# Performance work log

Hardware: AMD Instinct MI355X
Metric: run time of the kernel (lower is better)

## Reference

```python
import jax, jax.numpy as jnp
import numpy as np

B, A, UNITS, HID, T = 16, 256, 64, 64, 3


def setup_inputs() -> dict:
    key = jax.random.key(0)
    ks = jax.random.split(key, 16)
    x = jax.random.normal(ks[0], (B, A + 2, A), dtype=jnp.float32)
    # GNN message-passing weights (torch.randn in original)
    W0 = jax.random.normal(ks[1], (1, UNITS), dtype=jnp.float32)
    W1 = jax.random.normal(ks[2], (UNITS, UNITS), dtype=jnp.float32)
    W2 = jax.random.normal(ks[3], (UNITS, UNITS), dtype=jnp.float32)
    W3 = jax.random.normal(ks[4], (1, UNITS), dtype=jnp.float32)
    # fc_a: Linear(64,64)->ReLU->Linear(64,32)->ReLU->Linear(32,1); stored (in,out)
    s = lambda k, i, o: jax.random.uniform(k, (i, o), jnp.float32, -1, 1) / np.sqrt(i)
    sb = lambda k, i, o: jax.random.uniform(k, (o,), jnp.float32, -1, 1) / np.sqrt(i)
    a_w1, a_b1 = s(ks[5], UNITS, HID), sb(ks[6], UNITS, HID)
    a_w2, a_b2 = s(ks[7], HID, HID // 2), sb(ks[8], HID, HID // 2)
    a_w3, a_b3 = s(ks[9], HID // 2, 1), sb(ks[10], HID // 2, 1)
    # fc_v: Linear(64,64)->ReLU->Linear(64,1)
    v_w1, v_b1 = s(ks[11], UNITS, HID), sb(ks[12], UNITS, HID)
    v_w2, v_b2 = s(ks[13], HID, 1), sb(ks[14], HID, 1)
    return dict(x=x, W0=W0, W1=W1, W2=W2, W3=W3,
                a_w1=a_w1, a_b1=a_b1, a_w2=a_w2, a_b2=a_b2, a_w3=a_w3, a_b3=a_b3,
                v_w1=v_w1, v_b1=v_b1, v_w2=v_w2, v_b2=v_b2)


def reference(x, W0, W1, W2, W3,
              a_w1, a_b1, a_w2, a_b2, a_w3, a_b3,
              v_w1, v_b1, v_w2, v_b2):
    n_actions = x.shape[2]                       # A
    cur_sol = x[:, 0, :][..., None]              # [B, A, 1]
    mask = x[:, 1, :]                            # [B, A]
    weights = x[:, 2:n_actions + 2, :]           # [B, A, A]
    adjacent = (weights != 0).astype(jnp.float32)
    embedding = jnp.zeros((x.shape[0], n_actions, UNITS), dtype=jnp.float32)

    # e3 is loop-invariant in math, but original recomputes each step; keep T small python loop (faithful, T=3 static)
    for _ in range(T):
        e1 = cur_sol @ W0                                        # [B,A,1]@[1,U] -> [B,A,U]
        e2 = (adjacent @ embedding / n_actions) @ W1             # [B,A,U]
        # weights.reshape(B,A,A,1) @ W3(1,U) == outer-product broadcast
        e3_ = jnp.sum(jax.nn.relu(weights[..., None] * W3[0]), axis=2) / n_actions  # [B,A,U]
        e3 = e3_ @ W2
        embedding = jax.nn.relu(e1 + e2 + e3)

    # dueling heads
    h = jax.nn.relu(embedding @ a_w1 + a_b1)
    h = jax.nn.relu(h @ a_w2 + a_b2)
    out_a = (h @ a_w3 + a_b3)[..., 0]                            # [B, A]
    hv = jax.nn.relu(embedding @ v_w1 + v_b1)
    out_v = (hv @ v_w2 + v_b2)[..., 0]                           # [B, A]
    out_v = jnp.sum(out_v, axis=1, keepdims=True)                # [B, 1]
    output = out_v + (out_a - jnp.sum(out_a, axis=1, keepdims=True))
    output = output + mask * 10.0                                # hard_mask=False
    return output
```

## Files before the change

### kernel.cpp

```cpp
#include <hip/hip_runtime.h>


#define NB 16
#define NA 256
#define NU 64

__device__ __forceinline__ float reluf(float v) { return fmaxf(v, 0.f); }

__global__ __launch_bounds__(256) void k_fused(
    const float* __restrict__ x,
    const float* __restrict__ W0, const float* __restrict__ W1,
    const float* __restrict__ W2, const float* __restrict__ W3,
    const float* __restrict__ aw1, const float* __restrict__ ab1,
    const float* __restrict__ aw2, const float* __restrict__ ab2,
    const float* __restrict__ aw3, const float* __restrict__ ab3,
    const float* __restrict__ vw1, const float* __restrict__ vb1,
    const float* __restrict__ vw2, const float* __restrict__ vb2,
    float* __restrict__ oaw, float* __restrict__ partA, float* __restrict__ partV,
    unsigned int* __restrict__ cnt, float* __restrict__ embg,
    float* __restrict__ out)
{
    __shared__ float bufA[12384];
    __shared__ float W1s[4096];
    __shared__ unsigned long long zmsL[1024];
    __shared__ float poss[256], negs[256], css[256];
    __shared__ float W0s[64], P2s[64], N2s[64], Ssh[64], e2c[64];
    __shared__ float wpart[256], npart[256];
    __shared__ int   zrow[256];
    __shared__ int   zw[4];
    __shared__ float ab1s[64], vb1s[64], vw2s[64], ab2s[32], aw3s[32];
    __shared__ float ab3s[1], vb2s[1];
    __shared__ float soa[32], sov[32];
    __shared__ int   slast;

    const float invA = 1.0f / 256.0f;
    const int t = threadIdx.x;
    const int batch = blockIdx.x & 15;
    const int sub   = blockIdx.x >> 4;
    const int obase = sub * 32;
    float* aw1s = bufA;
    float* vw1s = bufA + 4096;
    float* aw2s = bufA + 8192;
    float* embs = bufA + 10304;

    #pragma unroll
    for (int k = 0; k < 4; ++k) {
        int idx = k * 1024 + t * 4;
        *(float4*)&aw1s[idx] = *(const float4*)&aw1[idx];
        *(float4*)&vw1s[idx] = *(const float4*)&vw1[idx];
        *(float4*)&W1s[idx]  = *(const float4*)&W1[idx];
    }
    #pragma unroll
    for (int k = 0; k < 8; ++k) {
        int idx = k * 256 + t;
        aw2s[(idx >> 5) * 33 + (idx & 31)] = aw2[idx];
    }
    if (t < 64) { W0s[t] = W0[t]; ab1s[t] = ab1[t]; vb1s[t] = vb1[t]; vw2s[t] = vw2[t]; }
    if (t >= 64 && t < 96) { ab2s[t - 64] = ab2[t - 64]; aw3s[t - 64] = aw3[t - 64]; }
    if (t == 96) { ab3s[0] = ab3[0]; vb2s[0] = vb2[0]; }

    {
        const int r4 = t >> 2, sub4 = t & 3;
        #pragma unroll
        for (int p = 0; p < 4; ++p) {
            int row = p * 64 + r4;
            const float* rowp = x + ((size_t)batch * 258 + 2 + row) * 256 + sub4 * 64;
            float pp = 0.f, nn = 0.f;
            int zf = 0;
            #pragma unroll
            for (int c = 0; c < 64; c += 4) {
                float4 v = *(const float4*)(rowp + c);
                pp += fmaxf(v.x, 0.f) + fmaxf(v.y, 0.f) + fmaxf(v.z, 0.f) + fmaxf(v.w, 0.f);
                nn += fminf(v.x, 0.f) + fminf(v.y, 0.f) + fminf(v.z, 0.f) + fminf(v.w, 0.f);
                zf |= (v.x == 0.f) | (v.y == 0.f) | (v.z == 0.f) | (v.w == 0.f);
            }
            pp += __shfl_xor(pp, 1); pp += __shfl_xor(pp, 2);
            nn += __shfl_xor(nn, 1); nn += __shfl_xor(nn, 2);
            zf |= __shfl_xor(zf, 1); zf |= __shfl_xor(zf, 2);
            if (sub4 == 0) { poss[row] = pp; negs[row] = nn; zrow[row] = zf; }
        }
        css[t] = x[(size_t)batch * 66048 + t];
    }

    {
        int j = t & 63, mg = t >> 6;
        float pa = 0.f, na = 0.f;
        #pragma unroll
        for (int k = 0; k < 16; ++k) {
            int m = mg * 16 + k;
            float w3 = W3[m];
            float w2 = W2[m * 64 + j];
            pa = fmaf(fmaxf(w3, 0.f), w2, pa);
            na = fmaf(fminf(w3, 0.f), w2, na);
        }
        wpart[mg * 64 + j] = pa;
        npart[mg * 64 + j] = na;
    }
    __syncthreads();
    {
        if (t < 64) {
            P2s[t] = wpart[t] + wpart[64 + t] + wpart[128 + t] + wpart[192 + t];
            N2s[t] = npart[t] + npart[64 + t] + npart[128 + t] + npart[192 + t];
        }
        int zf = zrow[t];
        unsigned long long ball = __ballot(zf != 0);
        if ((t & 63) == 0) zw[t >> 6] = (ball != 0ull) ? 1 : 0;
    }
    __syncthreads();
    const int dirty = zw[0] | zw[1] | zw[2] | zw[3];

    if (!dirty) {
        const int j = t & 63, rg = t >> 6;
        const float w0j = W0s[j], p2j = P2s[j], n2j = N2s[j];
        float c_j = 0.f;
        #pragma unroll
        for (int iter = 0; iter < 2; ++iter) {
            float s = 0.f;
            #pragma unroll 8
            for (int k = 0; k < 64; ++k) {
                int i = rg * 64 + k;
                s += reluf(fmaf(css[i], w0j, (poss[i] * p2j + negs[i] * n2j) * invA) + c_j);
            }
            wpart[rg * 64 + j] = s;
            __syncthreads();
            if (t < 64) {
                float S = wpart[t] + wpart[64 + t] + wpart[128 + t] + wpart[192 + t];
                Ssh[t] = S;
                float c = 0.f;
                #pragma unroll 8
                for (int m = 0; m < 64; ++m) c = fmaf(Ssh[m], W1s[m * 64 + t], c);
                e2c[t] = c * invA;
            }
            __syncthreads();
            c_j = e2c[j];
        }
        #pragma unroll
        for (int k = 0; k < 8; ++k) {
            int idx = k * 256 + t;
            int il = idx >> 6, j2 = idx & 63;
            int row = obase + il;
            embs[il * 65 + j2] = reluf(fmaf(css[row], W0s[j2],
                                 (poss[row] * P2s[j2] + negs[row] * N2s[j2]) * invA)
                                 + e2c[j2]);
        }
    } else {
        {
            const int r4 = t >> 2, sub4 = t & 3;
            #pragma unroll
            for (int p = 0; p < 4; ++p) {
                int row = p * 64 + r4;
                unsigned long long zm = 0ull;
                if (zrow[row]) {
                    const float* rowp = x + ((size_t)batch * 258 + 2 + row) * 256 + sub4 * 64;
                    for (int c = 0; c < 64; ++c)
                        if (rowp[c] == 0.f) zm |= 1ull << c;
                }
                zmsL[row * 4 + sub4] = zm;
            }
        }
        __syncthreads();
        float* eb0 = embg + (size_t)blockIdx.x * 32768;
        float* eb1 = eb0 + 16384;
        const int r4 = t >> 2, sub4 = t & 3, jb = sub4 * 16;
        #pragma unroll
        for (int p = 0; p < 4; ++p) {
            int row = p * 64 + r4;
            float cs = css[row], pi = poss[row], ni = negs[row];
            #pragma unroll
            for (int q = 0; q < 16; ++q) {
                int jj = jb + q;
                eb0[row * 64 + jj] = reluf(fmaf(cs, W0s[jj],
                                      (pi * P2s[jj] + ni * N2s[jj]) * invA));
            }
        }
        __syncthreads();
        float* cur = eb0; float* nxt = eb1;
        for (int it = 1; it <= 2; ++it) {
            {
                int j = t & 63, rg = t >> 6;
                float s = 0.f;
                for (int k = 0; k < 64; ++k) s += cur[(rg * 64 + k) * 64 + j];
                wpart[rg * 64 + j] = s;
            }
            __syncthreads();
            if (t < 64) {
                float S = wpart[t] + wpart[64 + t] + wpart[128 + t] + wpart[192 + t];
                Ssh[t] = S;
                float c = 0.f;
                for (int m = 0; m < 64; ++m) c = fmaf(Ssh[m], W1s[m * 64 + t], c);
                e2c[t] = c * invA;
            }
            __syncthreads();
            #pragma unroll
            for (int p = 0; p < 4; ++p) {
                int row = p * 64 + r4;
                float cs = css[row], pi = poss[row], ni = negs[row];
                float acc[16];
                #pragma unroll
                for (int q = 0; q < 16; ++q) {
                    int jj = jb + q;
                    acc[q] = fmaf(cs, W0s[jj], (pi * P2s[jj] + ni * N2s[jj]) * invA)
                             + e2c[jj];
                }
                if (zrow[row]) {
                    for (int wd = 0; wd < 4; ++wd) {
                        unsigned long long zm = zmsL[row * 4 + wd];
                        while (zm) {
                            int k = wd * 64 + __builtin_ctzll(zm);
                            zm &= zm - 1;
                            float corr[16];
                            #pragma unroll
                            for (int q = 0; q < 16; ++q) corr[q] = 0.f;
                            for (int m = 0; m < 64; ++m) {
                                float ebm = cur[k * 64 + m];
                                #pragma unroll
                                for (int q = 0; q < 16; ++q)
                                    corr[q] = fmaf(ebm, W1s[m * 64 + jb + q], corr[q]);
                            }
                            #pragma unroll
                            for (int q = 0; q < 16; ++q) acc[q] -= corr[q] * invA;
                        }
                    }
                }
                #pragma unroll
                for (int q = 0; q < 16; ++q)
                    nxt[row * 64 + jb + q] = reluf(acc[q]);
            }
            __syncthreads();
            float* tmp = cur; cur = nxt; nxt = tmp;
        }
        #pragma unroll
        for (int k = 0; k < 8; ++k) {
            int idx = k * 256 + t;
            int il = idx >> 6, j2 = idx & 63;
            embs[il * 65 + j2] = cur[(obase + il) * 64 + j2];
        }
    }
    __syncthreads();

    const int lr = t >> 3;
    const int jb = (t & 7) * 8;

    float h1[8], hv[8];
    #pragma unroll
    for (int q = 0; q < 8; ++q) { h1[q] = ab1s[jb + q]; hv[q] = vb1s[jb + q]; }

    for (int m = 0; m < 64; ++m) {
        float em = embs[lr * 65 + m];
        const float4 a0 = *(const float4*)&aw1s[m * 64 + jb];
        const float4 a1 = *(const float4*)&aw1s[m * 64 + jb + 4];
        const float4 b0 = *(const float4*)&vw1s[m * 64 + jb];
        const float4 b1 = *(const float4*)&vw1s[m * 64 + jb + 4];
        h1[0] = fmaf(em, a0.x, h1[0]); h1[1] = fmaf(em, a0.y, h1[1]);
        h1[2] = fmaf(em, a0.z, h1[2]); h1[3] = fmaf(em, a0.w, h1[3]);
        h1[4] = fmaf(em, a1.x, h1[4]); h1[5] = fmaf(em, a1.y, h1[5]);
        h1[6] = fmaf(em, a1.z, h1[6]); h1[7] = fmaf(em, a1.w, h1[7]);
        hv[0] = fmaf(em, b0.x, hv[0]); hv[1] = fmaf(em, b0.y, hv[1]);
        hv[2] = fmaf(em, b0.z, hv[2]); hv[3] = fmaf(em, b0.w, hv[3]);
        hv[4] = fmaf(em, b1.x, hv[4]); hv[5] = fmaf(em, b1.y, hv[5]);
        hv[6] = fmaf(em, b1.z, hv[6]); hv[7] = fmaf(em, b1.w, hv[7]);
    }

    float ovp = 0.f;
    #pragma unroll
    for (int q = 0; q < 8; ++q) {
        h1[q] = reluf(h1[q]);
        hv[q] = reluf(hv[q]);
        ovp = fmaf(hv[q], vw2s[jb + q], ovp);
    }
    ovp += __shfl_xor(ovp, 1); ovp += __shfl_xor(ovp, 2); ovp += __shfl_xor(ovp, 4);

    float h2p[32];
    #pragma unroll
    for (int j2 = 0; j2 < 32; ++j2) h2p[j2] = 0.f;
    #pragma unroll
    for (int q = 0; q < 8; ++q) {
        float h = h1[q];
        int rr = jb + q;
        #pragma unroll
        for (int j2 = 0; j2 < 32; ++j2) h2p[j2] = fmaf(h, aw2s[rr * 33 + j2], h2p[j2]);
    }
    #pragma unroll
    for (int j2 = 0; j2 < 32; ++j2) {
        float s = h2p[j2];
        s += __shfl_xor(s, 1); s += __shfl_xor(s, 2); s += __shfl_xor(s, 4);
        h2p[j2] = s;
    }

    if ((t & 7) == 0) {
        float oa = ab3s[0];
        #pragma unroll
        for (int j2 = 0; j2 < 32; ++j2)
            oa = fmaf(reluf(h2p[j2] + ab2s[j2]), aw3s[j2], oa);
        __hip_atomic_store(&oaw[batch * 256 + obase + lr], oa,
                           __ATOMIC_RELAXED, __HIP_MEMORY_SCOPE_AGENT);
        soa[lr] = oa;
        sov[lr] = ovp + vb2s[0];
    }
    __syncthreads();
    if (t < 32) {
        float a = soa[t], v = sov[t];
        a += __shfl_xor(a, 1); a += __shfl_xor(a, 2); a += __shfl_xor(a, 4);
        a += __shfl_xor(a, 8); a += __shfl_xor(a, 16);
        v += __shfl_xor(v, 1); v += __shfl_xor(v, 2); v += __shfl_xor(v, 4);
        v += __shfl_xor(v, 8); v += __shfl_xor(v, 16);
        if (t == 0) {
            __hip_atomic_store(&partA[blockIdx.x], a,
                               __ATOMIC_RELAXED, __HIP_MEMORY_SCOPE_AGENT);
            __hip_atomic_store(&partV[blockIdx.x], v,
                               __ATOMIC_RELAXED, __HIP_MEMORY_SCOPE_AGENT);
        }
    }

    __syncthreads();
    if (t == 0) {
        unsigned int old = __hip_atomic_fetch_add(&cnt[batch], 1u,
                               __ATOMIC_ACQ_REL, __HIP_MEMORY_SCOPE_AGENT);
        slast = (((old + 1u) & 7u) == 0u);
    }
    __syncthreads();
    if (slast) {
        float oa = __hip_atomic_load(&oaw[batch * 256 + t],
                                     __ATOMIC_RELAXED, __HIP_MEMORY_SCOPE_AGENT);
        float sA = 0.f, sV = 0.f;
        #pragma unroll
        for (int k = 0; k < 8; ++k) {
            sA += __hip_atomic_load(&partA[k * 16 + batch],
                                    __ATOMIC_RELAXED, __HIP_MEMORY_SCOPE_AGENT);
            sV += __hip_atomic_load(&partV[k * 16 + batch],
                                    __ATOMIC_RELAXED, __HIP_MEMORY_SCOPE_AGENT);
        }
        float mask = x[((size_t)batch * 258 + 1) * 256 + t];
        out[batch * 256 + t] = sV + oa - sA + mask * 10.0f;
    }
}

extern "C" void kernel_launch(void* const* d_in, const int* in_sizes, int n_in,
                              void* d_out, int out_size, void* d_ws, size_t ws_size,
                              hipStream_t stream)
{
    (void)in_sizes; (void)n_in; (void)out_size; (void)ws_size;
    const float* x   = (const float*)d_in[0];
    const float* W0  = (const float*)d_in[1];
    const float* W1  = (const float*)d_in[2];
    const float* W2  = (const float*)d_in[3];
    const float* W3  = (const float*)d_in[4];
    const float* aw1 = (const float*)d_in[5];
    const float* ab1 = (const float*)d_in[6];
    const float* aw2 = (const float*)d_in[7];
    const float* ab2 = (const float*)d_in[8];
    const float* aw3 = (const float*)d_in[9];
    const float* ab3 = (const float*)d_in[10];
    const float* vw1 = (const float*)d_in[11];
    const float* vb1 = (const float*)d_in[12];
    const float* vw2 = (const float*)d_in[13];
    const float* vb2 = (const float*)d_in[14];

    float* ws    = (float*)d_ws;
    float* oaw   = ws;
    float* partA = ws + 4096;
    float* partV = ws + 4224;
    unsigned int* cnt = (unsigned int*)(ws + 4352);
    float* embg  = ws + 8192;

    k_fused<<<128, 256, 0, stream>>>(x, W0, W1, W2, W3,
                                     aw1, ab1, aw2, ab2, aw3, ab3,
                                     vw1, vb1, vw2, vb2,
                                     oaw, partA, partV, cnt, embg, (float*)d_out);
}
```

Measured before the change: 28.86 us.

## Split row-statistics scan across blocks and exchange via global flags

```diff
diff --git a/kernel.cpp b/kernel.cpp
--- a/kernel.cpp
+++ b/kernel.cpp
@@ -1,9 +1,9 @@
 #include <hip/hip_runtime.h>
 
 
-#define NB 16
-#define NA 256
-#define NU 64
+#define MC  0x5F3A9C71u
+#define MD  0x5F3A9C72u
+#define MDN 0x5F3A9C73u
 
 __device__ __forceinline__ float reluf(float v) { return fmaxf(v, 0.f); }
 
@@ -16,71 +16,59 @@
     const float* __restrict__ aw3, const float* __restrict__ ab3,
     const float* __restrict__ vw1, const float* __restrict__ vb1,
     const float* __restrict__ vw2, const float* __restrict__ vb2,
-    float* __restrict__ oaw, float* __restrict__ partA, float* __restrict__ partV,
-    unsigned int* __restrict__ cnt, float* __restrict__ embg,
-    float* __restrict__ out)
+    float* __restrict__ oaw, float* __restrict__ ovv,
+    float* __restrict__ possg, float* __restrict__ negsg,
+    unsigned int* __restrict__ flagg, unsigned int* __restrict__ flag2,
+    float* __restrict__ embg, float* __restrict__ out)
 {
-    __shared__ float bufA[12384];
-    __shared__ float W1s[4096];
-    __shared__ unsigned long long zmsL[1024];
+    __shared__ float aw1s[4096], vw1s[4096], W1s[4096];
+    __shared__ float aw2s[64 * 36];
+    __shared__ float embsT[64 * 36];
     __shared__ float poss[256], negs[256], css[256];
     __shared__ float W0s[64], P2s[64], N2s[64], Ssh[64], e2c[64];
     __shared__ float wpart[256], npart[256];
-    __shared__ int   zrow[256];
-    __shared__ int   zw[4];
     __shared__ float ab1s[64], vb1s[64], vw2s[64], ab2s[32], aw3s[32];
-    __shared__ float ab3s[1], vb2s[1];
-    __shared__ float soa[32], sov[32];
-    __shared__ int   slast;
+    __shared__ float ab3s[1], vb2s[1], sov[32];
+    __shared__ int zw[4];
+    __shared__ unsigned int sflags[8];
+    __shared__ int zrow[256];
+    __shared__ unsigned long long zmsL[1024];
 
     const float invA = 1.0f / 256.0f;
     const int t = threadIdx.x;
     const int batch = blockIdx.x & 15;
     const int sub   = blockIdx.x >> 4;
     const int obase = sub * 32;
-    float* aw1s = bufA;
-    float* vw1s = bufA + 4096;
-    float* aw2s = bufA + 8192;
-    float* embs = bufA + 10304;
-
-    #pragma unroll
-    for (int k = 0; k < 4; ++k) {
-        int idx = k * 1024 + t * 4;
-        *(float4*)&aw1s[idx] = *(const float4*)&aw1[idx];
-        *(float4*)&vw1s[idx] = *(const float4*)&vw1[idx];
-        *(float4*)&W1s[idx]  = *(const float4*)&W1[idx];
-    }
-    #pragma unroll
-    for (int k = 0; k < 8; ++k) {
-        int idx = k * 256 + t;
-        aw2s[(idx >> 5) * 33 + (idx & 31)] = aw2[idx];
-    }
-    if (t < 64) { W0s[t] = W0[t]; ab1s[t] = ab1[t]; vb1s[t] = vb1[t]; vw2s[t] = vw2[t]; }
-    if (t >= 64 && t < 96) { ab2s[t - 64] = ab2[t - 64]; aw3s[t - 64] = aw3[t - 64]; }
-    if (t == 96) { ab3s[0] = ab3[0]; vb2s[0] = vb2[0]; }
 
     {
-        const int r4 = t >> 2, sub4 = t & 3;
+        int r8 = t >> 3, s8 = t & 7;
+        int grow = obase + r8;
+        const float* rowp = x + ((size_t)batch * 258 + 2 + grow) * 256 + s8 * 32;
+        float pp = 0.f, nn = 0.f, mn = 1e30f;
         #pragma unroll
-        for (int p = 0; p < 4; ++p) {
-            int row = p * 64 + r4;
-            const float* rowp = x + ((size_t)batch * 258 + 2 + row) * 256 + sub4 * 64;
-            float pp = 0.f, nn = 0.f;
-            int zf = 0;
-            #pragma unroll
-            for (int c = 0; c < 64; c += 4) {
-                float4 v = *(const float4*)(rowp + c);
-                pp += fmaxf(v.x, 0.f) + fmaxf(v.y, 0.f) + fmaxf(v.z, 0.f) + fmaxf(v.w, 0.f);
-                nn += fminf(v.x, 0.f) + fminf(v.y, 0.f) + fminf(v.z, 0.f) + fminf(v.w, 0.f);
-                zf |= (v.x == 0.f) | (v.y == 0.f) | (v.z == 0.f) | (v.w == 0.f);
-            }
-            pp += __shfl_xor(pp, 1); pp += __shfl_xor(pp, 2);
-            nn += __shfl_xor(nn, 1); nn += __shfl_xor(nn, 2);
-            zf |= __shfl_xor(zf, 1); zf |= __shfl_xor(zf, 2);
-            if (sub4 == 0) { poss[row] = pp; negs[row] = nn; zrow[row] = zf; }
-        }
-        css[t] = x[(size_t)batch * 66048 + t];
-    }
+        for (int c = 0; c < 32; c += 4) {
+            float4 v = *(const float4*)(rowp + c);
+            pp += fmaxf(v.x, 0.f) + fmaxf(v.y, 0.f) + fmaxf(v.z, 0.f) + fmaxf(v.w, 0.f);
+            nn += fminf(v.x, 0.f) + fminf(v.y, 0.f) + fminf(v.z, 0.f) + fminf(v.w, 0.f);
+            mn = fminf(mn, fminf(fminf(fabsf(v.x), fabsf(v.y)),
+                                 fminf(fabsf(v.z), fabsf(v.w))));
+        }
+        pp += __shfl_xor(pp, 1); pp += __shfl_xor(pp, 2); pp += __shfl_xor(pp, 4);
+        nn += __shfl_xor(nn, 1); nn += __shfl_xor(nn, 2); nn += __shfl_xor(nn, 4);
+        mn = fminf(mn, __shfl_xor(mn, 1));
+        mn = fminf(mn, __shfl_xor(mn, 2));
+        mn = fminf(mn, __shfl_xor(mn, 4));
+        if (s8 == 0) {
+            __hip_atomic_store(&possg[batch * 256 + grow], pp,
+                               __ATOMIC_RELAXED, __HIP_MEMORY_SCOPE_AGENT);
+            __hip_atomic_store(&negsg[batch * 256 + grow], nn,
+                               __ATOMIC_RELAXED, __HIP_MEMORY_SCOPE_AGENT);
+        }
+        int z = (s8 == 0 && mn == 0.f) ? 1 : 0;
+        unsigned long long b = __ballot(z);
+        if ((t & 63) == 0) zw[t >> 6] = (b != 0ull);
+    }
+    css[t] = x[(size_t)batch * 66048 + t];
 
     {
         int j = t & 63, mg = t >> 6;
@@ -97,17 +85,51 @@
         npart[mg * 64 + j] = na;
     }
     __syncthreads();
-    {
-        if (t < 64) {
-            P2s[t] = wpart[t] + wpart[64 + t] + wpart[128 + t] + wpart[192 + t];
-            N2s[t] = npart[t] + npart[64 + t] + npart[128 + t] + npart[192 + t];
-        }
-        int zf = zrow[t];
-        unsigned long long ball = __ballot(zf != 0);
-        if ((t & 63) == 0) zw[t >> 6] = (ball != 0ull) ? 1 : 0;
-    }
-    __syncthreads();
-    const int dirty = zw[0] | zw[1] | zw[2] | zw[3];
+    if (t == 0) {
+        unsigned int fv = (zw[0] | zw[1] | zw[2] | zw[3]) ? MD : MC;
+        __hip_atomic_store(&flagg[blockIdx.x], fv,
+                           __ATOMIC_RELEASE, __HIP_MEMORY_SCOPE_AGENT);
+    }
+    if (t < 64) {
+        P2s[t] = wpart[t] + wpart[64 + t] + wpart[128 + t] + wpart[192 + t];
+        N2s[t] = npart[t] + npart[64 + t] + npart[128 + t] + npart[192 + t];
+    }
+
+    #pragma unroll
+    for (int k = 0; k < 4; ++k) {
+        int idx = k * 1024 + t * 4;
+        *(float4*)&aw1s[idx] = *(const float4*)&aw1[idx];
+        *(float4*)&vw1s[idx] = *(const float4*)&vw1[idx];
+        *(float4*)&W1s[idx]  = *(const float4*)&W1[idx];
+    }
+    #pragma unroll
+    for (int k = 0; k < 8; ++k) {
+        int idx = k * 256 + t;
+        aw2s[(idx >> 5) * 36 + (idx & 31)] = aw2[idx];
+    }
+    if (t < 64) { W0s[t] = W0[t]; ab1s[t] = ab1[t]; vb1s[t] = vb1[t]; vw2s[t] = vw2[t]; }
+    if (t >= 64 && t < 96) { ab2s[t - 64] = ab2[t - 64]; aw3s[t - 64] = aw3[t - 64]; }
+    if (t == 96) { ab3s[0] = ab3[0]; vb2s[0] = vb2[0]; }
+
+    if (t < 8) {
+        const unsigned int* f = &flagg[t * 16 + batch];
+        unsigned int v = __hip_atomic_load(f, __ATOMIC_ACQUIRE, __HIP_MEMORY_SCOPE_AGENT);
+        while (v != MC && v != MD) {
+            __builtin_amdgcn_s_sleep(1);
+            v = __hip_atomic_load(f, __ATOMIC_ACQUIRE, __HIP_MEMORY_SCOPE_AGENT);
+        }
+        sflags[t] = v;
+    }
+    __syncthreads();
+    const int dirty = (sflags[0] == MD) | (sflags[1] == MD) | (sflags[2] == MD) |
+                      (sflags[3] == MD) | (sflags[4] == MD) | (sflags[5] == MD) |
+                      (sflags[6] == MD) | (sflags[7] == MD);
+
+    poss[t] = __hip_atomic_load(&possg[batch * 256 + t],
+                                __ATOMIC_RELAXED, __HIP_MEMORY_SCOPE_AGENT);
+    negs[t] = __hip_atomic_load(&negsg[batch * 256 + t],
+                                __ATOMIC_RELAXED, __HIP_MEMORY_SCOPE_AGENT);
+    __syncthreads();
 
     if (!dirty) {
         const int j = t & 63, rg = t >> 6;
@@ -134,14 +156,16 @@
             __syncthreads();
             c_j = e2c[j];
         }
-        #pragma unroll
-        for (int k = 0; k < 8; ++k) {
-            int idx = k * 256 + t;
-            int il = idx >> 6, j2 = idx & 63;
-            int row = obase + il;
-            embs[il * 65 + j2] = reluf(fmaf(css[row], W0s[j2],
-                                 (poss[row] * P2s[j2] + negs[row] * N2s[j2]) * invA)
-                                 + e2c[j2]);
+        {
+            int r = t & 31, mg = t >> 5;
+            int grow = obase + r;
+            float cs = css[grow], pi = poss[grow], ni = negs[grow];
+            #pragma unroll
+            for (int jj = 0; jj < 8; ++jj) {
+                int m = mg * 8 + jj;
+                embsT[m * 36 + r] = reluf(fmaf(cs, W0s[m],
+                                    (pi * P2s[m] + ni * N2s[m]) * invA) + e2c[m]);
+            }
         }
     } else {
         {
@@ -149,13 +173,14 @@
             #pragma unroll
             for (int p = 0; p < 4; ++p) {
                 int row = p * 64 + r4;
+                const float* rowp = x + ((size_t)batch * 258 + 2 + row) * 256 + sub4 * 64;
                 unsigned long long zm = 0ull;
-                if (zrow[row]) {
-                    const float* rowp = x + ((size_t)batch * 258 + 2 + row) * 256 + sub4 * 64;
-                    for (int c = 0; c < 64; ++c)
-                        if (rowp[c] == 0.f) zm |= 1ull << c;
-                }
+                for (int c = 0; c < 64; ++c)
+                    if (rowp[c] == 0.f) zm |= 1ull << c;
                 zmsL[row * 4 + sub4] = zm;
+                int zf = (zm != 0ull);
+                zf |= __shfl_xor(zf, 1); zf |= __shfl_xor(zf, 2);
+                if (sub4 == 0) zrow[row] = zf;
             }
         }
         __syncthreads();
@@ -229,107 +254,114 @@
             __syncthreads();
             float* tmp = cur; cur = nxt; nxt = tmp;
         }
-        #pragma unroll
-        for (int k = 0; k < 8; ++k) {
-            int idx = k * 256 + t;
-            int il = idx >> 6, j2 = idx & 63;
-            embs[il * 65 + j2] = cur[(obase + il) * 64 + j2];
-        }
-    }
-    __syncthreads();
-
-    const int lr = t >> 3;
-    const int jb = (t & 7) * 8;
-
-    float h1[8], hv[8];
+        for (int idx = t; idx < 2048; idx += 256) {
+            int r = idx & 31, m = idx >> 5;
+            embsT[m * 36 + r] = cur[(obase + r) * 64 + m];
+        }
+    }
+    __syncthreads();
+
+    const int cg  = t & 31;
+    const int rg4 = t >> 5;
+    float aA0x = 0.f, aA0y = 0.f, aA1x = 0.f, aA1y = 0.f;
+    float aA2x = 0.f, aA2y = 0.f, aA3x = 0.f, aA3y = 0.f;
+    float aV0x = 0.f, aV0y = 0.f, aV1x = 0.f, aV1y = 0.f;
+    float aV2x = 0.f, aV2y = 0.f, aV3x = 0.f, aV3y = 0.f;
+    for (int m = 0; m < 64; ++m) {
+        float4 em = *(const float4*)&embsT[m * 36 + rg4 * 4];
+        float2 a2 = *(const float2*)&aw1s[m * 64 + 2 * cg];
+        float2 v2 = *(const float2*)&vw1s[m * 64 + 2 * cg];
+        aA0x = fmaf(em.x, a2.x, aA0x); aA0y = fmaf(em.x, a2.y, aA0y);
+        aA1x = fmaf(em.y, a2.x, aA1x); aA1y = fmaf(em.y, a2.y, aA1y);
+        aA2x = fmaf(em.z, a2.x, aA2x); aA2y = fmaf(em.z, a2.y, aA2y);
+        aA3x = fmaf(em.w, a2.x, aA3x); aA3y = fmaf(em.w, a2.y, aA3y);
+        aV0x = fmaf(em.x, v2.x, aV0x); aV0y = fmaf(em.x, v2.y, aV0y);
+        aV1x = fmaf(em.y, v2.x, aV1x); aV1y = fmaf(em.y, v2.y, aV1y);
+        aV2x = fmaf(em.z, v2.x, aV2x); aV2y = fmaf(em.z, v2.y, aV2y);
+        aV3x = fmaf(em.w, v2.x, aV3x); aV3y = fmaf(em.w, v2.y, aV3y);
+    }
+    float wvx = vw2s[2 * cg], wvy = vw2s[2 * cg + 1];
+    float pv0 = fmaf(reluf(aV0x + vb1s[2 * cg]), wvx, reluf(aV0y + vb1s[2 * cg + 1]) * wvy);
+    float pv1 = fmaf(reluf(aV1x + vb1s[2 * cg]), wvx, reluf(aV1y + vb1s[2 * cg + 1]) * wvy);
+    float pv2 = fmaf(reluf(aV2x + vb1s[2 * cg]), wvx, reluf(aV2y + vb1s[2 * cg + 1]) * wvy);
+    float pv3 = fmaf(reluf(aV3x + vb1s[2 * cg]), wvx, reluf(aV3y + vb1s[2 * cg + 1]) * wvy);
     #pragma unroll
-    for (int q = 0; q < 8; ++q) { h1[q] = ab1s[jb + q]; hv[q] = vb1s[jb + q]; }
-
-    for (int m = 0; m < 64; ++m) {
-        float em = embs[lr * 65 + m];
-        const float4 a0 = *(const float4*)&aw1s[m * 64 + jb];
-        const float4 a1 = *(const float4*)&aw1s[m * 64 + jb + 4];
-        const float4 b0 = *(const float4*)&vw1s[m * 64 + jb];
-        const float4 b1 = *(const float4*)&vw1s[m * 64 + jb + 4];
-        h1[0] = fmaf(em, a0.x, h1[0]); h1[1] = fmaf(em, a0.y, h1[1]);
-        h1[2] = fmaf(em, a0.z, h1[2]); h1[3] = fmaf(em, a0.w, h1[3]);
-        h1[4] = fmaf(em, a1.x, h1[4]); h1[5] = fmaf(em, a1.y, h1[5]);
-        h1[6] = fmaf(em, a1.z, h1[6]); h1[7] = fmaf(em, a1.w, h1[7]);
-        hv[0] = fmaf(em, b0.x, hv[0]); hv[1] = fmaf(em, b0.y, hv[1]);
-        hv[2] = fmaf(em, b0.z, hv[2]); hv[3] = fmaf(em, b0.w, hv[3]);
-        hv[4] = fmaf(em, b1.x, hv[4]); hv[5] = fmaf(em, b1.y, hv[5]);
-        hv[6] = fmaf(em, b1.z, hv[6]); hv[7] = fmaf(em, b1.w, hv[7]);
-    }
-
-    float ovp = 0.f;
-    #pragma unroll
-    for (int q = 0; q < 8; ++q) {
-        h1[q] = reluf(h1[q]);
-        hv[q] = reluf(hv[q]);
-        ovp = fmaf(hv[q], vw2s[jb + q], ovp);
-    }
-    ovp += __shfl_xor(ovp, 1); ovp += __shfl_xor(ovp, 2); ovp += __shfl_xor(ovp, 4);
-
-    float h2p[32];
-    #pragma unroll
-    for (int j2 = 0; j2 < 32; ++j2) h2p[j2] = 0.f;
-    #pragma unroll
-    for (int q = 0; q < 8; ++q) {
-        float h = h1[q];
-        int rr = jb + q;
-        #pragma unroll
-        for (int j2 = 0; j2 < 32; ++j2) h2p[j2] = fmaf(h, aw2s[rr * 33 + j2], h2p[j2]);
-    }
-    #pragma unroll
-    for (int j2 = 0; j2 < 32; ++j2) {
-        float s = h2p[j2];
-        s += __shfl_xor(s, 1); s += __shfl_xor(s, 2); s += __shfl_xor(s, 4);
-        h2p[j2] = s;
-    }
-
-    if ((t & 7) == 0) {
-        float oa = ab3s[0];
-        #pragma unroll
-        for (int j2 = 0; j2 < 32; ++j2)
-            oa = fmaf(reluf(h2p[j2] + ab2s[j2]), aw3s[j2], oa);
-        __hip_atomic_store(&oaw[batch * 256 + obase + lr], oa,
+    for (int mk = 1; mk <= 16; mk <<= 1) {
+        pv0 += __shfl_xor(pv0, mk); pv1 += __shfl_xor(pv1, mk);
+        pv2 += __shfl_xor(pv2, mk); pv3 += __shfl_xor(pv3, mk);
+    }
+    float b0 = ab1s[2 * cg], b1 = ab1s[2 * cg + 1];
+    float h00 = reluf(aA0x + b0), h01 = reluf(aA0y + b1);
+    float h10 = reluf(aA1x + b0), h11 = reluf(aA1y + b1);
+    float h20 = reluf(aA2x + b0), h21 = reluf(aA2y + b1);
+    float h30 = reluf(aA3x + b0), h31 = reluf(aA3y + b1);
+    __syncthreads();
+    float* h1s = embsT;
+    *(float2*)&h1s[(rg4 * 4 + 0) * 68 + 2 * cg] = make_float2(h00, h01);
+    *(float2*)&h1s[(rg4 * 4 + 1) * 68 + 2 * cg] = make_float2(h10, h11);
+    *(float2*)&h1s[(rg4 * 4 + 2) * 68 + 2 * cg] = make_float2(h20, h21);
+    *(float2*)&h1s[(rg4 * 4 + 3) * 68 + 2 * cg] = make_float2(h30, h31);
+    if (cg == 0) {
+        sov[rg4 * 4 + 0] = pv0 + vb2s[0];
+        sov[rg4 * 4 + 1] = pv1 + vb2s[0];
+        sov[rg4 * 4 + 2] = pv2 + vb2s[0];
+        sov[rg4 * 4 + 3] = pv3 + vb2s[0];
+    }
+    __syncthreads();
+
+    {
+        int r = t >> 3, jg = t & 7;
+        float c0 = 0.f, c1 = 0.f, c2 = 0.f, c3 = 0.f;
+        for (int q = 0; q < 64; ++q) {
+            float h = h1s[r * 68 + q];
+            float4 w = *(const float4*)&aw2s[q * 36 + jg * 4];
+            c0 = fmaf(h, w.x, c0); c1 = fmaf(h, w.y, c1);
+            c2 = fmaf(h, w.z, c2); c3 = fmaf(h, w.w, c3);
+        }
+        float part = reluf(c0 + ab2s[jg * 4 + 0]) * aw3s[jg * 4 + 0];
+        part = fmaf(reluf(c1 + ab2s[jg * 4 + 1]), aw3s[jg * 4 + 1], part);
+        part = fmaf(reluf(c2 + ab2s[jg * 4 + 2]), aw3s[jg * 4 + 2], part);
+        part = fmaf(reluf(c3 + ab2s[jg * 4 + 3]), aw3s[jg * 4 + 3], part);
+        part += __shfl_xor(part, 1);
+        part += __shfl_xor(part, 2);
+        part += __shfl_xor(part, 4);
+        if (jg == 0)
+            __hip_atomic_store(&oaw[batch * 256 + obase + r], part + ab3s[0],
+                               __ATOMIC_RELAXED, __HIP_MEMORY_SCOPE_AGENT);
+    }
+    if (t < 32)
+        __hip_atomic_store(&ovv[batch * 256 + obase + t], sov[t],
                            __ATOMIC_RELAXED, __HIP_MEMORY_SCOPE_AGENT);
-        soa[lr] = oa;
-        sov[lr] = ovp + vb2s[0];
-    }
-    __syncthreads();
-    if (t < 32) {
-        float a = soa[t], v = sov[t];
-        a += __shfl_xor(a, 1); a += __shfl_xor(a, 2); a += __shfl_xor(a, 4);
-        a += __shfl_xor(a, 8); a += __shfl_xor(a, 16);
-        v += __shfl_xor(v, 1); v += __shfl_xor(v, 2); v += __shfl_xor(v, 4);
-        v += __shfl_xor(v, 8); v += __shfl_xor(v, 16);
-        if (t == 0) {
-            __hip_atomic_store(&partA[blockIdx.x], a,
-                               __ATOMIC_RELAXED, __HIP_MEMORY_SCOPE_AGENT);
-            __hip_atomic_store(&partV[blockIdx.x], v,
-                               __ATOMIC_RELAXED, __HIP_MEMORY_SCOPE_AGENT);
-        }
-    }
-
-    __syncthreads();
-    if (t == 0) {
-        unsigned int old = __hip_atomic_fetch_add(&cnt[batch], 1u,
-                               __ATOMIC_ACQ_REL, __HIP_MEMORY_SCOPE_AGENT);
-        slast = (((old + 1u) & 7u) == 0u);
-    }
-    __syncthreads();
-    if (slast) {
+    __syncthreads();
+    if (t == 0)
+        __hip_atomic_store(&flag2[blockIdx.x], MDN,
+                           __ATOMIC_RELEASE, __HIP_MEMORY_SCOPE_AGENT);
+
+    if (sub == 0) {
+        if (t < 8) {
+            const unsigned int* f = &flag2[t * 16 + batch];
+            unsigned int v = __hip_atomic_load(f, __ATOMIC_ACQUIRE,
+                                               __HIP_MEMORY_SCOPE_AGENT);
+            while (v != MDN) {
+                __builtin_amdgcn_s_sleep(1);
+                v = __hip_atomic_load(f, __ATOMIC_ACQUIRE, __HIP_MEMORY_SCOPE_AGENT);
+            }
+        }
+        __syncthreads();
         float oa = __hip_atomic_load(&oaw[batch * 256 + t],
                                      __ATOMIC_RELAXED, __HIP_MEMORY_SCOPE_AGENT);
-        float sA = 0.f, sV = 0.f;
+        float ov = __hip_atomic_load(&ovv[batch * 256 + t],
+                                     __ATOMIC_RELAXED, __HIP_MEMORY_SCOPE_AGENT);
+        float sa = oa, sv = ov;
         #pragma unroll
-        for (int k = 0; k < 8; ++k) {
-            sA += __hip_atomic_load(&partA[k * 16 + batch],
-                                    __ATOMIC_RELAXED, __HIP_MEMORY_SCOPE_AGENT);
-            sV += __hip_atomic_load(&partV[k * 16 + batch],
-                                    __ATOMIC_RELAXED, __HIP_MEMORY_SCOPE_AGENT);
-        }
+        for (int mk = 1; mk <= 32; mk <<= 1) {
+            sa += __shfl_xor(sa, mk);
+            sv += __shfl_xor(sv, mk);
+        }
+        if ((t & 63) == 0) { wpart[t >> 6] = sa; npart[t >> 6] = sv; }
+        __syncthreads();
+        float sA = wpart[0] + wpart[1] + wpart[2] + wpart[3];
+        float sV = npart[0] + npart[1] + npart[2] + npart[3];
         float mask = x[((size_t)batch * 258 + 1) * 256 + t];
         out[batch * 256 + t] = sV + oa - sA + mask * 10.0f;
     }
@@ -356,15 +388,18 @@
     const float* vw2 = (const float*)d_in[13];
     const float* vb2 = (const float*)d_in[14];
 
-    float* ws    = (float*)d_ws;
+    float* ws = (float*)d_ws;
     float* oaw   = ws;
-    float* partA = ws + 4096;
-    float* partV = ws + 4224;
-    unsigned int* cnt = (unsigned int*)(ws + 4352);
-    float* embg  = ws + 8192;
+    float* ovv   = ws + 4096;
+    float* possg = ws + 8192;
+    float* negsg = ws + 12288;
+    unsigned int* flagg = (unsigned int*)(ws + 16384);
+    unsigned int* flag2 = (unsigned int*)(ws + 16512);
+    float* embg  = ws + 16640;
 
     k_fused<<<128, 256, 0, stream>>>(x, W0, W1, W2, W3,
                                      aw1, ab1, aw2, ab2, aw3, ab3,
                                      vw1, vb1, vw2, vb2,
-                                     oaw, partA, partV, cnt, embg, (float*)d_out);
+                                     oaw, ovv, possg, negsg, flagg, flag2,
+                                     embg, (float*)d_out);
 }
```

Measured after the change: 23.96 us. 1.2x faster.
